# Kernel tuning notes

Hardware: AMD Instinct MI355X
Metric: run time of the kernel (lower is better)

The kernel has to match this reference:

```python
import jax, jax.numpy as jnp
import numpy as np

NUM_NODES = 50000
NUM_EDGES = 800000
DIM = 96


def setup_inputs() -> dict:
    key = jax.random.key(0)
    k1, k2, k3, k4, k5, k6 = jax.random.split(key, 6)
    x = jax.random.normal(k1, (NUM_NODES, DIM), dtype=jnp.float32)
    edge_index = jax.random.randint(k2, (2, NUM_EDGES), 0, NUM_NODES, dtype=jnp.int64)
    s = 1.0 / np.sqrt(DIM)
    W_self = jax.random.uniform(k3, (DIM, DIM), dtype=jnp.float32, minval=-s, maxval=s)
    b_self = jax.random.uniform(k4, (DIM,), dtype=jnp.float32, minval=-s, maxval=s)
    W_neigh = jax.random.uniform(k5, (DIM, DIM), dtype=jnp.float32, minval=-s, maxval=s)
    b_neigh = jax.random.uniform(k6, (DIM,), dtype=jnp.float32, minval=-s, maxval=s)
    return {"x": x, "edge_index": edge_index, "W_self": W_self, "b_self": b_self,
            "W_neigh": W_neigh, "b_neigh": b_neigh}


def reference(x, edge_index, W_self, b_self, W_neigh, b_neigh):
    source, target = edge_index[0], edge_index[1]
    # scatter-add of gathered source features into target rows
    aggregated = jax.ops.segment_sum(x[source], target, num_segments=NUM_NODES)  # [N, D]
    degree = jax.ops.segment_sum(jnp.ones((NUM_EDGES,), dtype=x.dtype), target,
                                 num_segments=NUM_NODES)[:, None]  # [N, 1]
    neighbor_mean = aggregated / jnp.maximum(degree, 1.0)
    # nn.Linear applies x @ W.T + b
    return x @ W_self.T + b_self + neighbor_mean @ W_neigh.T + b_neigh
```

## Files before the change

kernel.cpp:

```cpp
#include <hip/hip_runtime.h>
#include <hip/hip_bf16.h>

#define N_NODES 50000
#define N_EDGES 800000
#define DIM 96
#define NPART 256
#define PSZ 196
#define NBINBLK 196
#define BINCAP 48
#define BPP (NBINBLK * BINCAP)
#define CAP 4096
#define NROWBLK 1563


typedef unsigned int uint;
typedef unsigned short u16;

__device__ __forceinline__ u16 f2bf(float f) {
    __hip_bfloat16 h = __float2bfloat16(f);
    return *reinterpret_cast<u16*>(&h);
}
__device__ __forceinline__ float bf2f(u16 u) {
    return __uint_as_float(((uint)u) << 16);
}
__device__ __forceinline__ int pdiv(int t) { return (int)(((uint)t * 85599u) >> 24); }

__global__ __launch_bounds__(256) void packbin_k(
    const float* __restrict__ x, const int* __restrict__ ei,
    u16* __restrict__ xbf, signed char* __restrict__ xq, float* __restrict__ scales,
    uint* __restrict__ part_edges, int* __restrict__ counts)
{
    __shared__ uint bins[NPART * BINCAP];
    __shared__ int  bcnt[NPART];
    const int tid = threadIdx.x;

    if (blockIdx.x >= NBINBLK) {
        const int rb = blockIdx.x - NBINBLK;
        const int row = rb * 32 + (tid >> 3);
        if (row < N_NODES) {
            const int l = tid & 7;
            const float* rp = x + (size_t)row * DIM + l * 12;
            float4 f0 = *reinterpret_cast<const float4*>(rp);
            float4 f1 = *reinterpret_cast<const float4*>(rp + 4);
            float4 f2 = *reinterpret_cast<const float4*>(rp + 8);
            float v[12] = {f0.x, f0.y, f0.z, f0.w,
                           f1.x, f1.y, f1.z, f1.w,
                           f2.x, f2.y, f2.z, f2.w};
            float amax = 0.f;
#pragma unroll
            for (int k = 0; k < 12; k++) amax = fmaxf(amax, fabsf(v[k]));
#pragma unroll
            for (int mk = 1; mk < 8; mk <<= 1)
                amax = fmaxf(amax, __shfl_xor(amax, mk, 8));
            const float inv = (amax > 0.f) ? 127.0f / amax : 0.f;
            const float sc  = (amax > 0.f) ? amax * (1.0f / 127.0f) : 0.f;

            ushort4 h0, h1, h2;
            h0.x = f2bf(v[0]);  h0.y = f2bf(v[1]);  h0.z = f2bf(v[2]);  h0.w = f2bf(v[3]);
            h1.x = f2bf(v[4]);  h1.y = f2bf(v[5]);  h1.z = f2bf(v[6]);  h1.w = f2bf(v[7]);
            h2.x = f2bf(v[8]);  h2.y = f2bf(v[9]);  h2.z = f2bf(v[10]); h2.w = f2bf(v[11]);
            u16* hb = xbf + (size_t)row * DIM + l * 12;
            *reinterpret_cast<ushort4*>(hb)     = h0;
            *reinterpret_cast<ushort4*>(hb + 4) = h1;
            *reinterpret_cast<ushort4*>(hb + 8) = h2;

            uint w[3];
#pragma unroll
            for (int g = 0; g < 3; g++) {
                int q0 = __float2int_rn(v[g * 4 + 0] * inv);
                int q1 = __float2int_rn(v[g * 4 + 1] * inv);
                int q2 = __float2int_rn(v[g * 4 + 2] * inv);
                int q3 = __float2int_rn(v[g * 4 + 3] * inv);
                w[g] = (uint)(q0 & 0xFF) | ((uint)(q1 & 0xFF) << 8) |
                       ((uint)(q2 & 0xFF) << 16) | ((uint)(q3 & 0xFF) << 24);
            }
            uint* qb = reinterpret_cast<uint*>(xq + (size_t)row * DIM) + l * 3;
            qb[0] = w[0]; qb[1] = w[1]; qb[2] = w[2];
            if (l == 0) scales[row] = sc;
        }
        return;
    }

    for (int i = tid; i < NPART; i += 256) bcnt[i] = 0;
    __syncthreads();

    const int e0 = blockIdx.x * 4096 + tid * 16;
    if (e0 + 16 <= N_EDGES) {
#pragma unroll
        for (int j = 0; j < 4; j++) {
            int4 s = *reinterpret_cast<const int4*>(ei + e0 + j * 4);
            int4 t = *reinterpret_cast<const int4*>(ei + N_EDGES + e0 + j * 4);
            int ss[4] = {s.x, s.y, s.z, s.w};
            int tt[4] = {t.x, t.y, t.z, t.w};
#pragma unroll
            for (int k = 0; k < 4; k++) {
                int p = pdiv(tt[k]);
                int local = tt[k] - p * PSZ;
                int slot = atomicAdd(&bcnt[p], 1);
                if (slot < BINCAP)
                    bins[p * BINCAP + slot] = ((uint)local << 16) | (uint)ss[k];
            }
        }
    } else {
        for (int j = 0; j < 16; j++) {
            int e = e0 + j;
            if (e < N_EDGES) {
                int sv = ei[e];
                int tv = ei[N_EDGES + e];
                int p = pdiv(tv);
                int local = tv - p * PSZ;
                int slot = atomicAdd(&bcnt[p], 1);
                if (slot < BINCAP)
                    bins[p * BINCAP + slot] = ((uint)local << 16) | (uint)sv;
            }
        }
    }
    __syncthreads();

    for (int p = tid; p < NPART; p += 256)
        counts[p * NBINBLK + blockIdx.x] = min(bcnt[p], BINCAP);

    for (int i = tid; i < NPART * BINCAP; i += 256) {
        int p = i / BINCAP;
        int s = i - p * BINCAP;
        if (s < bcnt[p])
            part_edges[(size_t)p * BPP + blockIdx.x * BINCAP + s] = bins[i];
    }
}

__device__ __forceinline__ void wave_scan256(int* a, int tid) {
    if (tid < 64) {
        int v0 = a[tid * 4], v1 = a[tid * 4 + 1], v2 = a[tid * 4 + 2], v3 = a[tid * 4 + 3];
        int s01 = v0 + v1;
        int s = s01 + v2 + v3;
        int inc = s;
#pragma unroll
        for (int off = 1; off < 64; off <<= 1) {
            int n = __shfl_up(inc, off, 64);
            if (tid >= off) inc += n;
        }
        int base = inc - s;
        a[tid * 4]     = base + v0;
        a[tid * 4 + 1] = base + s01;
        a[tid * 4 + 2] = base + s01 + v2;
        a[tid * 4 + 3] = base + s;
    }
}

union QV { uint2 u; signed char b[8]; };

__global__ __launch_bounds__(1024) void fused_k(
    const u16* __restrict__ xbf,
    const signed char* __restrict__ xq, const float* __restrict__ scales,
    const uint* __restrict__ part_edges,
    const int* __restrict__ counts,
    const float* __restrict__ Wself, const float* __restrict__ bself,
    const float* __restrict__ Wneigh, const float* __restrict__ bneigh,
    float* __restrict__ out)
{
    using short8 = __attribute__((ext_vector_type(8))) short;
    using f32x4  = __attribute__((ext_vector_type(4))) float;

    __shared__ u16   Axm[208 * 200];
    __shared__ short Bb[96 * 200];
    __shared__ uint  recs[CAP];
    __shared__ u16   ssrc[CAP];
    __shared__ int   bc[256];
    __shared__ int   csc[256];
    __shared__ int   hist[256];
    __shared__ int   cur[256];

    const int tid = threadIdx.x;
    const int p = blockIdx.x;
    const int node0 = p * PSZ;

    uint pr[10];
    {
        const uint* pe = part_edges + (size_t)p * BPP;
#pragma unroll
        for (int k = 0; k < 9; k++) pr[k] = pe[tid + k * 1024];
        pr[9] = (tid < BPP - 9216) ? pe[9216 + tid] : 0u;
    }

    if (tid < 256) {
        int v = (tid < NBINBLK) ? counts[p * NBINBLK + tid] : 0;
        bc[tid] = v;
        csc[tid] = v;
        cur[tid] = 0;
    }

    for (int idx = tid; idx < 96 * 96; idx += 1024) {
        int j = idx / 96;
        int k = idx - j * 96;
        Bb[j * 200 + k]      = (short)f2bf(Wself[idx]);
        Bb[j * 200 + 96 + k] = (short)f2bf(Wneigh[idx]);
    }

    for (int i = tid; i < PSZ * 12; i += 1024) {
        int n = i / 12, t = i - n * 12;
        int node = node0 + n;
        short8 v = (short8)0;
        if (node < N_NODES)
            v = *reinterpret_cast<const short8*>(xbf + (size_t)node * DIM + t * 8);
        *reinterpret_cast<short8*>(&Axm[n * 200 + t * 8]) = v;
    }
    __syncthreads();

    wave_scan256(csc, tid);
    __syncthreads();
    int m = csc[255]; if (m > CAP) m = CAP;

#pragma unroll
    for (int k = 0; k < 10; k++) {
        int i = tid + k * 1024;
        if (i < BPP) {
            int b = i / BINCAP;
            int s = i - b * BINCAP;
            if (s < bc[b]) {
                int dst = csc[b] - bc[b] + s;
                if (dst < CAP) {
                    uint r = pr[k];
                    recs[dst] = r;
                    atomicAdd(&cur[r >> 16], 1);
                }
            }
        }
    }
    __syncthreads();

    if (tid < 256) hist[tid] = cur[tid];
    __syncthreads();
    wave_scan256(hist, tid);
    __syncthreads();
    if (tid < 256) cur[tid] = hist[tid] - cur[tid];
    __syncthreads();

    for (int i = tid; i < m; i += 1024) {
        uint r = recs[i];
        int pos = atomicAdd(&cur[r >> 16], 1);
        ssrc[pos] = (u16)(r & 0xFFFF);
    }
    __syncthreads();

    if (tid < 1020) {
        const int g = tid / 12;
        const int l = tid - g * 12;
        const int l8b = l * 8;
        for (int r = g; r < PSZ; r += 85) {
            int end = hist[r];
            int beg = (r > 0) ? hist[r - 1] : 0;
            float a0 = 0.f, a1 = 0.f, a2 = 0.f, a3 = 0.f;
            float a4 = 0.f, a5 = 0.f, a6 = 0.f, a7 = 0.f;
            int i = beg;
            for (; i + 3 < end; i += 4) {
                int s0 = ssrc[i], s1 = ssrc[i + 1], s2 = ssrc[i + 2], s3 = ssrc[i + 3];
                QV q0, q1, q2, q3;
                q0.u = *reinterpret_cast<const uint2*>(xq + (size_t)s0 * DIM + l8b);
                q1.u = *reinterpret_cast<const uint2*>(xq + (size_t)s1 * DIM + l8b);
                q2.u = *reinterpret_cast<const uint2*>(xq + (size_t)s2 * DIM + l8b);
                q3.u = *reinterpret_cast<const uint2*>(xq + (size_t)s3 * DIM + l8b);
                float c0 = scales[s0], c1 = scales[s1], c2 = scales[s2], c3 = scales[s3];
                a0 += c0 * (float)q0.b[0] + c1 * (float)q1.b[0]
                    + c2 * (float)q2.b[0] + c3 * (float)q3.b[0];
                a1 += c0 * (float)q0.b[1] + c1 * (float)q1.b[1]
                    + c2 * (float)q2.b[1] + c3 * (float)q3.b[1];
                a2 += c0 * (float)q0.b[2] + c1 * (float)q1.b[2]
                    + c2 * (float)q2.b[2] + c3 * (float)q3.b[2];
                a3 += c0 * (float)q0.b[3] + c1 * (float)q1.b[3]
                    + c2 * (float)q2.b[3] + c3 * (float)q3.b[3];
                a4 += c0 * (float)q0.b[4] + c1 * (float)q1.b[4]
                    + c2 * (float)q2.b[4] + c3 * (float)q3.b[4];
                a5 += c0 * (float)q0.b[5] + c1 * (float)q1.b[5]
                    + c2 * (float)q2.b[5] + c3 * (float)q3.b[5];
                a6 += c0 * (float)q0.b[6] + c1 * (float)q1.b[6]
                    + c2 * (float)q2.b[6] + c3 * (float)q3.b[6];
                a7 += c0 * (float)q0.b[7] + c1 * (float)q1.b[7]
                    + c2 * (float)q2.b[7] + c3 * (float)q3.b[7];
            }
            for (; i < end; i++) {
                int s = ssrc[i];
                QV q;
                q.u = *reinterpret_cast<const uint2*>(xq + (size_t)s * DIM + l8b);
                float c = scales[s];
                a0 += c * (float)q.b[0]; a1 += c * (float)q.b[1];
                a2 += c * (float)q.b[2]; a3 += c * (float)q.b[3];
                a4 += c * (float)q.b[4]; a5 += c * (float)q.b[5];
                a6 += c * (float)q.b[6]; a7 += c * (float)q.b[7];
            }
            float inv = (end > beg) ? 1.0f / (float)(end - beg) : 0.f;
            ushort4 o0, o1;
            o0.x = f2bf(a0 * inv); o0.y = f2bf(a1 * inv);
            o0.z = f2bf(a2 * inv); o0.w = f2bf(a3 * inv);
            o1.x = f2bf(a4 * inv); o1.y = f2bf(a5 * inv);
            o1.z = f2bf(a6 * inv); o1.w = f2bf(a7 * inv);
            u16* ob = &Axm[r * 200 + 96 + l8b];
            *reinterpret_cast<ushort4*>(ob)     = o0;
            *reinterpret_cast<ushort4*>(ob + 4) = o1;
        }
    }
    __syncthreads();

    const int wave = tid >> 6;
    const int lane = tid & 63;
    const int quad = lane >> 4;
    const int m16  = lane & 15;

    if (wave < 13) {
        const int rloc = wave * 16;
        f32x4 acc[6];
#pragma unroll
        for (int nt = 0; nt < 6; nt++) acc[nt] = (f32x4){0.f, 0.f, 0.f, 0.f};

#pragma unroll
        for (int kt = 0; kt < 6; kt++) {
            short8 a = *reinterpret_cast<const short8*>(
                &Axm[(rloc + m16) * 200 + kt * 32 + quad * 8]);
#pragma unroll
            for (int nt = 0; nt < 6; nt++) {
                short8 b = *reinterpret_cast<const short8*>(
                    &Bb[(nt * 16 + m16) * 200 + kt * 32 + quad * 8]);
                acc[nt] = __builtin_amdgcn_mfma_f32_16x16x32_bf16(a, b, acc[nt], 0, 0, 0);
            }
        }

#pragma unroll
        for (int nt = 0; nt < 6; nt++) {
            int col = nt * 16 + m16;
            float bias = bself[col] + bneigh[col];
#pragma unroll
            for (int reg = 0; reg < 4; reg++) {
                int rl = rloc + quad * 4 + reg;
                int row = node0 + rl;
                if (rl < PSZ && row < N_NODES)
                    out[(size_t)row * DIM + col] = acc[nt][reg] + bias;
            }
        }
    }
}

extern "C" void kernel_launch(void* const* d_in, const int* in_sizes, int n_in,
                              void* d_out, int out_size, void* d_ws, size_t ws_size,
                              hipStream_t stream) {
    const float* x      = (const float*)d_in[0];
    const int*   ei     = (const int*)d_in[1];
    const float* Wself  = (const float*)d_in[2];
    const float* bself  = (const float*)d_in[3];
    const float* Wneigh = (const float*)d_in[4];
    const float* bneigh = (const float*)d_in[5];
    float* out = (float*)d_out;

    uint* part_edges = (uint*)d_ws;
    int*  counts     = (int*)(part_edges + (size_t)NPART * BPP);
    u16*  xbf        = (u16*)(counts + NPART * NBINBLK);
    signed char* xq  = (signed char*)(xbf + (size_t)N_NODES * DIM);
    float* scales    = (float*)(xq + (size_t)N_NODES * DIM);

    packbin_k<<<NBINBLK + NROWBLK, 256, 0, stream>>>(
        x, ei, xbf, xq, scales, part_edges, counts);
    fused_k<<<NPART, 1024, 0, stream>>>(
        xbf, xq, scales, part_edges, counts, Wself, bself, Wneigh, bneigh, out);
}
```

Measured before the change: 119.5 us.

## Sort edges by target directly from registers, dropping compaction pass and extra scans

Replaces the two-stage compaction (bin-count scan into a recs buffer, then histogram scan and scatter) with a direct counting sort. Records still held in registers are histogrammed, then one wave scans while the other threads convert weights to bf16, then the registers are scattered into ssrc. This removes a shared buffer, one scan and several barriers. The CAP overflow check now applies to per-node positions, which changes behaviour only if more than CAP edges land in one partition.

```diff
diff --git a/kernel.cpp b/kernel.cpp
--- a/kernel.cpp
+++ b/kernel.cpp
@@ -128,25 +128,6 @@
     }
 }
 
-__device__ __forceinline__ void wave_scan256(int* a, int tid) {
-    if (tid < 64) {
-        int v0 = a[tid * 4], v1 = a[tid * 4 + 1], v2 = a[tid * 4 + 2], v3 = a[tid * 4 + 3];
-        int s01 = v0 + v1;
-        int s = s01 + v2 + v3;
-        int inc = s;
-#pragma unroll
-        for (int off = 1; off < 64; off <<= 1) {
-            int n = __shfl_up(inc, off, 64);
-            if (tid >= off) inc += n;
-        }
-        int base = inc - s;
-        a[tid * 4]     = base + v0;
-        a[tid * 4 + 1] = base + s01;
-        a[tid * 4 + 2] = base + s01 + v2;
-        a[tid * 4 + 3] = base + s;
-    }
-}
-
 union QV { uint2 u; signed char b[8]; };
 
 __global__ __launch_bounds__(1024) void fused_k(
@@ -163,10 +144,8 @@
 
     __shared__ u16   Axm[208 * 200];
     __shared__ short Bb[96 * 200];
-    __shared__ uint  recs[CAP];
     __shared__ u16   ssrc[CAP];
     __shared__ int   bc[256];
-    __shared__ int   csc[256];
     __shared__ int   hist[256];
     __shared__ int   cur[256];
 
@@ -185,15 +164,7 @@
     if (tid < 256) {
         int v = (tid < NBINBLK) ? counts[p * NBINBLK + tid] : 0;
         bc[tid] = v;
-        csc[tid] = v;
         cur[tid] = 0;
-    }
-
-    for (int idx = tid; idx < 96 * 96; idx += 1024) {
-        int j = idx / 96;
-        int k = idx - j * 96;
-        Bb[j * 200 + k]      = (short)f2bf(Wself[idx]);
-        Bb[j * 200 + 96 + k] = (short)f2bf(Wneigh[idx]);
     }
 
     for (int i = tid; i < PSZ * 12; i += 1024) {
@@ -206,9 +177,47 @@
     }
     __syncthreads();
 
-    wave_scan256(csc, tid);
-    __syncthreads();
-    int m = csc[255]; if (m > CAP) m = CAP;
+#pragma unroll
+    for (int k = 0; k < 10; k++) {
+        int i = tid + k * 1024;
+        if (i < BPP) {
+            int b = i / BINCAP;
+            int s = i - b * BINCAP;
+            if (s < bc[b])
+                atomicAdd(&cur[pr[k] >> 16], 1);
+        }
+    }
+    __syncthreads();
+
+    if (tid < 64) {
+        int t4 = tid * 4;
+        int v0 = cur[t4], v1 = cur[t4 + 1], v2 = cur[t4 + 2], v3 = cur[t4 + 3];
+        int s01 = v0 + v1;
+        int s = s01 + v2 + v3;
+        int inc = s;
+#pragma unroll
+        for (int off = 1; off < 64; off <<= 1) {
+            int n = __shfl_up(inc, off, 64);
+            if (tid >= off) inc += n;
+        }
+        int base = inc - s;
+        hist[t4]     = base + v0;
+        hist[t4 + 1] = base + s01;
+        hist[t4 + 2] = base + s01 + v2;
+        hist[t4 + 3] = base + s;
+        cur[t4]      = base;
+        cur[t4 + 1]  = base + v0;
+        cur[t4 + 2]  = base + s01;
+        cur[t4 + 3]  = base + s01 + v2;
+    } else {
+        for (int idx = tid - 64; idx < 96 * 96; idx += 960) {
+            int j = idx / 96;
+            int k = idx - j * 96;
+            Bb[j * 200 + k]      = (short)f2bf(Wself[idx]);
+            Bb[j * 200 + 96 + k] = (short)f2bf(Wneigh[idx]);
+        }
+    }
+    __syncthreads();
 
 #pragma unroll
     for (int k = 0; k < 10; k++) {
@@ -217,28 +226,12 @@
             int b = i / BINCAP;
             int s = i - b * BINCAP;
             if (s < bc[b]) {
-                int dst = csc[b] - bc[b] + s;
-                if (dst < CAP) {
-                    uint r = pr[k];
-                    recs[dst] = r;
-                    atomicAdd(&cur[r >> 16], 1);
-                }
-            }
-        }
-    }
-    __syncthreads();
-
-    if (tid < 256) hist[tid] = cur[tid];
-    __syncthreads();
-    wave_scan256(hist, tid);
-    __syncthreads();
-    if (tid < 256) cur[tid] = hist[tid] - cur[tid];
-    __syncthreads();
-
-    for (int i = tid; i < m; i += 1024) {
-        uint r = recs[i];
-        int pos = atomicAdd(&cur[r >> 16], 1);
-        ssrc[pos] = (u16)(r & 0xFFFF);
+                uint r = pr[k];
+                int pos = atomicAdd(&cur[r >> 16], 1);
+                if (pos < CAP)
+                    ssrc[pos] = (u16)(r & 0xFFFF);
+            }
+        }
     }
     __syncthreads();
 
```

Result: no change. 120.6 us (+0.9%).

## Drop bf16 copy of x and balance row aggregation with atomic work queue

Applied to the files above, without the earlier changes.

Removes the intermediate bf16 copy of x written by the pack kernel; the fused kernel now reads fp32 x directly and converts to bf16 while staging its tile into shared memory. This saves a full-size global write plus reread. The neighbor aggregation switches from a static row stride across 85 groups to a dynamic shared-memory atomic row counter, with 5 groups of 12 lanes per wave, to balance rows of uneven degree. The cost is that each wave now leaves 4 of its 64 lanes idle, and each row fetch adds an atomic and a shuffle.

```diff
diff --git a/kernel.cpp b/kernel.cpp
--- a/kernel.cpp
+++ b/kernel.cpp
@@ -27,7 +27,7 @@
 
 __global__ __launch_bounds__(256) void packbin_k(
     const float* __restrict__ x, const int* __restrict__ ei,
-    u16* __restrict__ xbf, signed char* __restrict__ xq, float* __restrict__ scales,
+    signed char* __restrict__ xq, float* __restrict__ scales,
     uint* __restrict__ part_edges, int* __restrict__ counts)
 {
     __shared__ uint bins[NPART * BINCAP];
@@ -55,15 +55,6 @@
             const float inv = (amax > 0.f) ? 127.0f / amax : 0.f;
             const float sc  = (amax > 0.f) ? amax * (1.0f / 127.0f) : 0.f;
 
-            ushort4 h0, h1, h2;
-            h0.x = f2bf(v[0]);  h0.y = f2bf(v[1]);  h0.z = f2bf(v[2]);  h0.w = f2bf(v[3]);
-            h1.x = f2bf(v[4]);  h1.y = f2bf(v[5]);  h1.z = f2bf(v[6]);  h1.w = f2bf(v[7]);
-            h2.x = f2bf(v[8]);  h2.y = f2bf(v[9]);  h2.z = f2bf(v[10]); h2.w = f2bf(v[11]);
-            u16* hb = xbf + (size_t)row * DIM + l * 12;
-            *reinterpret_cast<ushort4*>(hb)     = h0;
-            *reinterpret_cast<ushort4*>(hb + 4) = h1;
-            *reinterpret_cast<ushort4*>(hb + 8) = h2;
-
             uint w[3];
 #pragma unroll
             for (int g = 0; g < 3; g++) {
@@ -150,7 +141,7 @@
 union QV { uint2 u; signed char b[8]; };
 
 __global__ __launch_bounds__(1024) void fused_k(
-    const u16* __restrict__ xbf,
+    const float* __restrict__ x,
     const signed char* __restrict__ xq, const float* __restrict__ scales,
     const uint* __restrict__ part_edges,
     const int* __restrict__ counts,
@@ -169,6 +160,7 @@
     __shared__ int   csc[256];
     __shared__ int   hist[256];
     __shared__ int   cur[256];
+    __shared__ int   rowcur;
 
     const int tid = threadIdx.x;
     const int p = blockIdx.x;
@@ -188,6 +180,7 @@
         csc[tid] = v;
         cur[tid] = 0;
     }
+    if (tid == 0) rowcur = 0;
 
     for (int idx = tid; idx < 96 * 96; idx += 1024) {
         int j = idx / 96;
@@ -200,8 +193,15 @@
         int n = i / 12, t = i - n * 12;
         int node = node0 + n;
         short8 v = (short8)0;
-        if (node < N_NODES)
-            v = *reinterpret_cast<const short8*>(xbf + (size_t)node * DIM + t * 8);
+        if (node < N_NODES) {
+            const float* rp = x + (size_t)node * DIM + t * 8;
+            float4 f0 = *reinterpret_cast<const float4*>(rp);
+            float4 f1 = *reinterpret_cast<const float4*>(rp + 4);
+            v[0] = (short)f2bf(f0.x); v[1] = (short)f2bf(f0.y);
+            v[2] = (short)f2bf(f0.z); v[3] = (short)f2bf(f0.w);
+            v[4] = (short)f2bf(f1.x); v[5] = (short)f2bf(f1.y);
+            v[6] = (short)f2bf(f1.z); v[7] = (short)f2bf(f1.w);
+        }
         *reinterpret_cast<short8*>(&Axm[n * 200 + t * 8]) = v;
     }
     __syncthreads();
@@ -242,60 +242,67 @@
     }
     __syncthreads();
 
-    if (tid < 1020) {
-        const int g = tid / 12;
-        const int l = tid - g * 12;
+    {
+        const int lane = tid & 63;
+        const int sub = lane / 12;
+        const int l = lane - sub * 12;
         const int l8b = l * 8;
-        for (int r = g; r < PSZ; r += 85) {
-            int end = hist[r];
-            int beg = (r > 0) ? hist[r - 1] : 0;
-            float a0 = 0.f, a1 = 0.f, a2 = 0.f, a3 = 0.f;
-            float a4 = 0.f, a5 = 0.f, a6 = 0.f, a7 = 0.f;
-            int i = beg;
-            for (; i + 3 < end; i += 4) {
-                int s0 = ssrc[i], s1 = ssrc[i + 1], s2 = ssrc[i + 2], s3 = ssrc[i + 3];
-                QV q0, q1, q2, q3;
-                q0.u = *reinterpret_cast<const uint2*>(xq + (size_t)s0 * DIM + l8b);
-                q1.u = *reinterpret_cast<const uint2*>(xq + (size_t)s1 * DIM + l8b);
-                q2.u = *reinterpret_cast<const uint2*>(xq + (size_t)s2 * DIM + l8b);
-                q3.u = *reinterpret_cast<const uint2*>(xq + (size_t)s3 * DIM + l8b);
-                float c0 = scales[s0], c1 = scales[s1], c2 = scales[s2], c3 = scales[s3];
-                a0 += c0 * (float)q0.b[0] + c1 * (float)q1.b[0]
-                    + c2 * (float)q2.b[0] + c3 * (float)q3.b[0];
-                a1 += c0 * (float)q0.b[1] + c1 * (float)q1.b[1]
-                    + c2 * (float)q2.b[1] + c3 * (float)q3.b[1];
-                a2 += c0 * (float)q0.b[2] + c1 * (float)q1.b[2]
-                    + c2 * (float)q2.b[2] + c3 * (float)q3.b[2];
-                a3 += c0 * (float)q0.b[3] + c1 * (float)q1.b[3]
-                    + c2 * (float)q2.b[3] + c3 * (float)q3.b[3];
-                a4 += c0 * (float)q0.b[4] + c1 * (float)q1.b[4]
-                    + c2 * (float)q2.b[4] + c3 * (float)q3.b[4];
-                a5 += c0 * (float)q0.b[5] + c1 * (float)q1.b[5]
-                    + c2 * (float)q2.b[5] + c3 * (float)q3.b[5];
-                a6 += c0 * (float)q0.b[6] + c1 * (float)q1.b[6]
-                    + c2 * (float)q2.b[6] + c3 * (float)q3.b[6];
-                a7 += c0 * (float)q0.b[7] + c1 * (float)q1.b[7]
-                    + c2 * (float)q2.b[7] + c3 * (float)q3.b[7];
-            }
-            for (; i < end; i++) {
-                int s = ssrc[i];
-                QV q;
-                q.u = *reinterpret_cast<const uint2*>(xq + (size_t)s * DIM + l8b);
-                float c = scales[s];
-                a0 += c * (float)q.b[0]; a1 += c * (float)q.b[1];
-                a2 += c * (float)q.b[2]; a3 += c * (float)q.b[3];
-                a4 += c * (float)q.b[4]; a5 += c * (float)q.b[5];
-                a6 += c * (float)q.b[6]; a7 += c * (float)q.b[7];
-            }
-            float inv = (end > beg) ? 1.0f / (float)(end - beg) : 0.f;
-            ushort4 o0, o1;
-            o0.x = f2bf(a0 * inv); o0.y = f2bf(a1 * inv);
-            o0.z = f2bf(a2 * inv); o0.w = f2bf(a3 * inv);
-            o1.x = f2bf(a4 * inv); o1.y = f2bf(a5 * inv);
-            o1.z = f2bf(a6 * inv); o1.w = f2bf(a7 * inv);
-            u16* ob = &Axm[r * 200 + 96 + l8b];
-            *reinterpret_cast<ushort4*>(ob)     = o0;
-            *reinterpret_cast<ushort4*>(ob + 4) = o1;
+        if (sub < 5) {
+            while (true) {
+                int r;
+                if (l == 0) r = atomicAdd(&rowcur, 1);
+                r = __shfl(r, sub * 12, 64);
+                if (r >= PSZ) break;
+                int end = hist[r];
+                int beg = (r > 0) ? hist[r - 1] : 0;
+                float a0 = 0.f, a1 = 0.f, a2 = 0.f, a3 = 0.f;
+                float a4 = 0.f, a5 = 0.f, a6 = 0.f, a7 = 0.f;
+                int i = beg;
+                for (; i + 3 < end; i += 4) {
+                    int s0 = ssrc[i], s1 = ssrc[i + 1], s2 = ssrc[i + 2], s3 = ssrc[i + 3];
+                    QV q0, q1, q2, q3;
+                    q0.u = *reinterpret_cast<const uint2*>(xq + (size_t)s0 * DIM + l8b);
+                    q1.u = *reinterpret_cast<const uint2*>(xq + (size_t)s1 * DIM + l8b);
+                    q2.u = *reinterpret_cast<const uint2*>(xq + (size_t)s2 * DIM + l8b);
+                    q3.u = *reinterpret_cast<const uint2*>(xq + (size_t)s3 * DIM + l8b);
+                    float c0 = scales[s0], c1 = scales[s1], c2 = scales[s2], c3 = scales[s3];
+                    a0 += c0 * (float)q0.b[0] + c1 * (float)q1.b[0]
+                        + c2 * (float)q2.b[0] + c3 * (float)q3.b[0];
+                    a1 += c0 * (float)q0.b[1] + c1 * (float)q1.b[1]
+                        + c2 * (float)q2.b[1] + c3 * (float)q3.b[1];
+                    a2 += c0 * (float)q0.b[2] + c1 * (float)q1.b[2]
+                        + c2 * (float)q2.b[2] + c3 * (float)q3.b[2];
+                    a3 += c0 * (float)q0.b[3] + c1 * (float)q1.b[3]
+                        + c2 * (float)q2.b[3] + c3 * (float)q3.b[3];
+                    a4 += c0 * (float)q0.b[4] + c1 * (float)q1.b[4]
+                        + c2 * (float)q2.b[4] + c3 * (float)q3.b[4];
+                    a5 += c0 * (float)q0.b[5] + c1 * (float)q1.b[5]
+                        + c2 * (float)q2.b[5] + c3 * (float)q3.b[5];
+                    a6 += c0 * (float)q0.b[6] + c1 * (float)q1.b[6]
+                        + c2 * (float)q2.b[6] + c3 * (float)q3.b[6];
+                    a7 += c0 * (float)q0.b[7] + c1 * (float)q1.b[7]
+                        + c2 * (float)q2.b[7] + c3 * (float)q3.b[7];
+                }
+                for (; i < end; i++) {
+                    int s = ssrc[i];
+                    QV q;
+                    q.u = *reinterpret_cast<const uint2*>(xq + (size_t)s * DIM + l8b);
+                    float c = scales[s];
+                    a0 += c * (float)q.b[0]; a1 += c * (float)q.b[1];
+                    a2 += c * (float)q.b[2]; a3 += c * (float)q.b[3];
+                    a4 += c * (float)q.b[4]; a5 += c * (float)q.b[5];
+                    a6 += c * (float)q.b[6]; a7 += c * (float)q.b[7];
+                }
+                float inv = (end > beg) ? 1.0f / (float)(end - beg) : 0.f;
+                ushort4 o0, o1;
+                o0.x = f2bf(a0 * inv); o0.y = f2bf(a1 * inv);
+                o0.z = f2bf(a2 * inv); o0.w = f2bf(a3 * inv);
+                o1.x = f2bf(a4 * inv); o1.y = f2bf(a5 * inv);
+                o1.z = f2bf(a6 * inv); o1.w = f2bf(a7 * inv);
+                u16* ob = &Axm[r * 200 + 96 + l8b];
+                *reinterpret_cast<ushort4*>(ob)     = o0;
+                *reinterpret_cast<ushort4*>(ob + 4) = o1;
+            }
         }
     }
     __syncthreads();
@@ -351,12 +358,11 @@
 
     uint* part_edges = (uint*)d_ws;
     int*  counts     = (int*)(part_edges + (size_t)NPART * BPP);
-    u16*  xbf        = (u16*)(counts + NPART * NBINBLK);
-    signed char* xq  = (signed char*)(xbf + (size_t)N_NODES * DIM);
+    signed char* xq  = (signed char*)(counts + NPART * NBINBLK);
     float* scales    = (float*)(xq + (size_t)N_NODES * DIM);
 
     packbin_k<<<NBINBLK + NROWBLK, 256, 0, stream>>>(
-        x, ei, xbf, xq, scales, part_edges, counts);
+        x, ei, xq, scales, part_edges, counts);
     fused_k<<<NPART, 1024, 0, stream>>>(
-        xbf, xq, scales, part_edges, counts, Wself, bself, Wneigh, bneigh, out);
-}
+        x, xq, scales, part_edges, counts, Wself, bself, Wneigh, bneigh, out);
+}
```

Result: no change. 119.7 us (+0.1%).
